# Kernel optimization log

Measured on AMD Instinct MI355X. Metric: run time of the kernel, lower is better.

Reference implementation:

```python
import jax, jax.numpy as jnp
import numpy as np

# 4-neighbor cross stencil deltas from CONNECTION_FLAGS_3x3_small
DELTAS = ((-1, 0), (0, -1), (0, 1), (1, 0))


def setup_inputs() -> dict:
    key = jax.random.key(0)
    k1, k2, k3 = jax.random.split(key, 3)
    B, G, C, H, W = 4, 8, 32, 128, 128
    patchs = jax.random.normal(k1, (B, G, C, H, W), dtype=jnp.float32)
    edge_weights = jax.random.uniform(k2, (B, G, 4, H, W), dtype=jnp.float32)
    node_degree = jax.random.uniform(k3, (B, G, H, W), dtype=jnp.float32)
    return {"patchs": patchs, "edge_weights": edge_weights, "node_degree": node_degree}


def _gather_neighbors(x):
    # x: [B, GC, H, W] -> [B, GC, 4, H, W] with replicate padding (torch 'replicate' == jnp 'edge')
    B, GC, H, W = x.shape
    xp = jnp.pad(x, ((0, 0), (0, 0), (1, 1), (1, 1)), mode='edge')
    nbrs = [xp[:, :, 1 + dh:1 + dh + H, 1 + dw:1 + dw + W] for dh, dw in DELTAS]
    return jnp.stack(nbrs, axis=2)


def reference(patchs, edge_weights, node_degree):
    # patchs: [B, G, C, H, W]; edge_weights: [B, G, 4, H, W]; node_degree unused in forward
    B, G, C, H, W = patchs.shape
    x = patchs.reshape(B, G * C, H, W)
    nbrs = _gather_neighbors(x).reshape(B, G, C, 4, H, W)
    Wx = jnp.einsum('bgcehw,bgehw->bgchw', nbrs, edge_weights)
    return patchs - Wx
```

## Files before the change

### kernel.cpp

```cpp
#include <hip/hip_runtime.h>


#define GLR_HW 16384

typedef float fvec4 __attribute__((ext_vector_type(4)));

__global__ __launch_bounds__(512, 4) void glr_fwd_kernel(
    const float* __restrict__ patchs,
    const float* __restrict__ ew,
    float* __restrict__ out)
{
    __shared__ float4 sw[2048];

    const int t  = threadIdx.x;
    const int w4 = t & 31;
    const int ch = t >> 5;

    const int b     = blockIdx.x;
    const int q     = b >> 3;
    const int bg    = (b & 7) + ((q >> 4) << 3);
    const int rr    = q & 15;
    const int strip = rr >> 1;
    const int hf    = rr & 1;

    const int r0 = strip << 4;
    const int w  = w4 << 2;

    const int plane = (bg << 5) + (hf << 4) + ch;
    const float* __restrict__ P = patchs + (size_t)plane * GLR_HW + w;
    float*       __restrict__ O = out    + (size_t)plane * GLR_HW + w;

    const float* __restrict__ EW =
        ew + (size_t)bg * 4 * GLR_HW + ((r0 + ch) << 7) + w;
    float4 wreg[4];
    #pragma unroll
    for (int k = 0; k < 4; ++k)
        wreg[k] = *(const float4*)(EW + k * GLR_HW);

    float4 reg[18];
    #pragma unroll
    for (int i = 0; i < 18; ++i) {
        int r = r0 + i - 1;
        r = (r < 0) ? 0 : (r > 127 ? 127 : r);
        reg[i] = *(const float4*)(P + (r << 7));
    }

    #pragma unroll
    for (int k = 0; k < 4; ++k)
        sw[t + (k << 9)] = wreg[k];
    __syncthreads();

    const bool atL = (w4 == 0);
    const bool atR = (w4 == 31);

    #pragma unroll
    for (int i = 0; i < 16; ++i) {
        const float4 up  = reg[i];
        const float4 cur = reg[i + 1];
        const float4 dn  = reg[i + 2];

        const int si = (i << 5) + w4;
        const float4 e0 = sw[si];
        const float4 e1 = sw[512 + si];
        const float4 e2 = sw[1024 + si];
        const float4 e3 = sw[1536 + si];

        float lf = __shfl_up(cur.w, 1);
        float rg = __shfl_down(cur.x, 1);
        if (atL) lf = cur.x;
        if (atR) rg = cur.w;

        fvec4 o;
        o.x = cur.x - (up.x * e0.x + lf    * e1.x + cur.y * e2.x + dn.x * e3.x);
        o.y = cur.y - (up.y * e0.y + cur.x * e1.y + cur.z * e2.y + dn.y * e3.y);
        o.z = cur.z - (up.z * e0.z + cur.y * e1.z + cur.w * e2.z + dn.z * e3.z);
        o.w = cur.w - (up.w * e0.w + cur.z * e1.w + rg    * e2.w + dn.w * e3.w);

        *(fvec4*)(O + ((r0 + i) << 7)) = o;
    }
}

extern "C" void kernel_launch(void* const* d_in, const int* in_sizes, int n_in,
                              void* d_out, int out_size, void* d_ws, size_t ws_size,
                              hipStream_t stream) {
    const float* patchs = (const float*)d_in[0];
    const float* ew     = (const float*)d_in[1];
    float* out = (float*)d_out;

    glr_fwd_kernel<<<512, 512, 0, stream>>>(patchs, ew, out);
}
```

Baseline: 122.6 us.

## Replace shared-memory edge-weight staging with per-row register prefetch and smaller blocks

Removes the LDS buffer and the __syncthreads: each thread now loads the four edge-weight vectors per row straight from global memory, double-buffered two rows ahead in registers. Blocks shrink to 256 threads covering 8 channels, with 1024 blocks instead of 512. Each block re-reads edge weights per channel, so global/L2 traffic for weights rises 8x, in exchange for no barrier and no LDS traffic.

```diff
diff --git a/kernel.cpp b/kernel.cpp
--- a/kernel.cpp
+++ b/kernel.cpp
@@ -5,37 +5,37 @@
 
 typedef float fvec4 __attribute__((ext_vector_type(4)));
 
-__global__ __launch_bounds__(512, 4) void glr_fwd_kernel(
+__global__ __launch_bounds__(256, 4) void glr_fwd_kernel(
     const float* __restrict__ patchs,
     const float* __restrict__ ew,
     float* __restrict__ out)
 {
-    __shared__ float4 sw[2048];
-
     const int t  = threadIdx.x;
     const int w4 = t & 31;
     const int ch = t >> 5;
 
     const int b     = blockIdx.x;
     const int q     = b >> 3;
-    const int bg    = (b & 7) + ((q >> 4) << 3);
-    const int rr    = q & 15;
-    const int strip = rr >> 1;
-    const int hf    = rr & 1;
+    const int bg    = (b & 7) + ((q >> 5) << 3);
+    const int rr    = q & 31;
+    const int strip = rr >> 2;
+    const int cg    = rr & 3;
 
     const int r0 = strip << 4;
     const int w  = w4 << 2;
 
-    const int plane = (bg << 5) + (hf << 4) + ch;
+    const int plane = (bg << 5) + (cg << 3) + ch;
     const float* __restrict__ P = patchs + (size_t)plane * GLR_HW + w;
     float*       __restrict__ O = out    + (size_t)plane * GLR_HW + w;
+    const float* __restrict__ EW = ew + (size_t)bg * 4 * GLR_HW + w;
 
-    const float* __restrict__ EW =
-        ew + (size_t)bg * 4 * GLR_HW + ((r0 + ch) << 7) + w;
-    float4 wreg[4];
+    float4 ewp[2][4];
     #pragma unroll
     for (int k = 0; k < 4; ++k)
-        wreg[k] = *(const float4*)(EW + k * GLR_HW);
+        ewp[0][k] = *(const float4*)(EW + k * GLR_HW + ((r0 + 0) << 7));
+    #pragma unroll
+    for (int k = 0; k < 4; ++k)
+        ewp[1][k] = *(const float4*)(EW + k * GLR_HW + ((r0 + 1) << 7));
 
     float4 reg[18];
     #pragma unroll
@@ -44,11 +44,6 @@
         r = (r < 0) ? 0 : (r > 127 ? 127 : r);
         reg[i] = *(const float4*)(P + (r << 7));
     }
-
-    #pragma unroll
-    for (int k = 0; k < 4; ++k)
-        sw[t + (k << 9)] = wreg[k];
-    __syncthreads();
 
     const bool atL = (w4 == 0);
     const bool atR = (w4 == 31);
@@ -59,11 +54,10 @@
         const float4 cur = reg[i + 1];
         const float4 dn  = reg[i + 2];
 
-        const int si = (i << 5) + w4;
-        const float4 e0 = sw[si];
-        const float4 e1 = sw[512 + si];
-        const float4 e2 = sw[1024 + si];
-        const float4 e3 = sw[1536 + si];
+        const float4 e0 = ewp[i & 1][0];
+        const float4 e1 = ewp[i & 1][1];
+        const float4 e2 = ewp[i & 1][2];
+        const float4 e3 = ewp[i & 1][3];
 
         float lf = __shfl_up(cur.w, 1);
         float rg = __shfl_down(cur.x, 1);
@@ -77,6 +71,13 @@
         o.w = cur.w - (up.w * e0.w + cur.z * e1.w + rg    * e2.w + dn.w * e3.w);
 
         *(fvec4*)(O + ((r0 + i) << 7)) = o;
+
+        if (i < 14) {
+            #pragma unroll
+            for (int k = 0; k < 4; ++k)
+                ewp[i & 1][k] =
+                    *(const float4*)(EW + k * GLR_HW + ((r0 + i + 2) << 7));
+        }
     }
 }
 
@@ -87,5 +88,5 @@
     const float* ew     = (const float*)d_in[1];
     float* out = (float*)d_out;
 
-    glr_fwd_kernel<<<512, 512, 0, stream>>>(patchs, ew, out);
+    glr_fwd_kernel<<<1024, 256, 0, stream>>>(patchs, ew, out);
 }
```

Measured after the change: 125.4 us. 1.02x slower.
